# Kernel optimization log

Hardware: AMD Instinct MI355X
Metric: run time of the kernel (lower is better)

## Reference

```python
import jax, jax.numpy as jnp
import numpy as np
import math

B, NQ, HID = 1, 512, 4096
H, KVH, D = 32, 8, 128
NPRE, TOPK = 4096, 64
NREP = H // KVH


def _rope_tables(nq, d, base=10000.0):
    inv_freq = 1.0 / (base ** (np.arange(0, d, 2, dtype=np.float32) / d))
    freqs = np.outer(np.arange(nq, dtype=np.float32), inv_freq)  # [nq, d/2]
    emb = np.concatenate([freqs, freqs], axis=-1)                # [nq, d]
    return jnp.asarray(np.cos(emb))[None], jnp.asarray(np.sin(emb))[None]


def setup_inputs() -> dict:
    key = jax.random.key(0)
    ks = jax.random.split(key, 8)
    cos, sin = _rope_tables(NQ, D)
    wscale = 0.02
    return {
        "hidden_states": jax.random.normal(ks[0], (B, NQ, HID), jnp.float32),
        "cos": cos.astype(jnp.float32),
        "sin": sin.astype(jnp.float32),
        "prefix_key": jax.random.normal(ks[1], (B, KVH, NPRE, D), jnp.float32),
        "prefix_value": jax.random.normal(ks[2], (B, KVH, NPRE, D), jnp.float32),
        "Wq": jax.random.normal(ks[3], (HID, H * D), jnp.float32) * wscale,
        "Wk": jax.random.normal(ks[4], (HID, KVH * D), jnp.float32) * wscale,
        "Wv": jax.random.normal(ks[5], (HID, KVH * D), jnp.float32) * wscale,
        "Wo": jax.random.normal(ks[6], (H * D, HID), jnp.float32) * wscale,
    }


def _rotate_half(x):
    x1, x2 = jnp.split(x, 2, axis=-1)
    return jnp.concatenate([-x2, x1], axis=-1)


def _apply_rope(x, cos, sin):
    # x: [B, h, N, D]; cos/sin: [B, N, D] -> unsqueeze head dim (HF convention)
    c, s = cos[:, None], sin[:, None]
    return x * c + _rotate_half(x) * s


def _repeat_kv(x, n_rep):
    # [B, kvH, N, D] -> [B, kvH*n_rep, N, D] (repeat_interleave on head dim)
    b, kvh, n, d = x.shape
    return jnp.broadcast_to(x[:, :, None], (b, kvh, n_rep, n, d)).reshape(b, kvh * n_rep, n, d)


def reference(hidden_states, cos, sin, prefix_key, prefix_value, Wq, Wk, Wv, Wo):
    inv_sqrt_d = 1.0 / math.sqrt(D)

    q = (hidden_states @ Wq).reshape(B, NQ, H, D).transpose(0, 2, 1, 3)    # [B,H,Nq,D]
    k = (hidden_states @ Wk).reshape(B, NQ, KVH, D).transpose(0, 2, 1, 3)  # [B,kvH,Nq,D]
    v = (hidden_states @ Wv).reshape(B, NQ, KVH, D).transpose(0, 2, 1, 3)

    q = _apply_rope(q, cos, sin)
    k = _apply_rope(k, cos, sin)

    sk = _repeat_kv(k, NREP).reshape(B * H, NQ, D)            # suffix keys
    sv = _repeat_kv(v, NREP).reshape(B * H, NQ, D)            # suffix values
    pk = _repeat_kv(prefix_key, NREP).reshape(B * H, NPRE, D)  # FAISS DB keys (exact IP index)
    pv = _repeat_kv(prefix_value, NREP).reshape(B * H, NPRE, D)
    qf = q.reshape(B * H, NQ, D)

    # --- exact top-k inner-product search over prefix (== FAISS IndexFlatIP), scaled by 1/sqrt(D)
    prefix_scores = jnp.einsum('bnd,bmd->bnm', qf, pk) * inv_sqrt_d        # [BH,Nq,Npre]
    topk_values, topk_indices = jax.lax.top_k(prefix_scores, TOPK)         # [BH,Nq,k]

    topk_exp = jnp.exp(topk_values)
    topk_exp_sums = topk_exp.sum(axis=-1)                                  # [BH,Nq]

    # --- dense causal suffix attention (unnormalized, exp without max-shift, as in source)
    score_dense = jnp.einsum('bnd,bmd->bnm', qf, sk) * inv_sqrt_d          # [BH,Nq,Nq]
    causal = jnp.tril(jnp.ones((NQ, NQ), bool))
    score_dense = jnp.where(causal[None], score_dense, -jnp.inf)
    dense_exp = jnp.exp(score_dense)
    dense_exp_sums = dense_exp.sum(axis=-1)                                # [BH,Nq]

    denom = (topk_exp_sums + dense_exp_sums)[..., None]                    # shared softmax denom
    attn_topk = topk_exp / denom                                           # [BH,Nq,k]
    attn_dense = dense_exp / denom                                         # [BH,Nq,Nq]

    # --- sparse (COO) matmul with prefix values == gather + weighted sum
    bh_idx = jnp.arange(B * H)[:, None, None]
    gathered_pv = pv[bh_idx, topk_indices]                                 # [BH,Nq,k,D]
    xhat = jnp.einsum('bnk,bnkd->bnd', attn_topk, gathered_pv)
    xhat = xhat + attn_dense @ sv                                          # [BH,Nq,D]

    out = xhat.reshape(B, H, NQ, D).transpose(0, 2, 1, 3).reshape(B, NQ, H * D)
    return out @ Wo                                                        # [B,Nq,HID]
```

## Files before the change

### kernel.cpp

```cpp
#include <hip/hip_runtime.h>

#define DEV static __device__ __forceinline__

typedef _Float16 f16;
typedef __attribute__((ext_vector_type(8))) _Float16 f16x8;
typedef __attribute__((ext_vector_type(4))) _Float16 f16x4;
typedef __attribute__((ext_vector_type(4))) float    f32x4;

#define SCALE_QK 0.08838834764831845f

DEV float u2f(unsigned x){ union{unsigned u; float f;} c; c.u = x; return c.f; }

DEV void gload16(const f16* g, f16* l){
  __builtin_amdgcn_global_load_lds((const __attribute__((address_space(1))) void*)g,
                                   (__attribute__((address_space(3))) void*)l, 16, 0, 0);
}

template<int BM, int BN>
DEV void gemm_core3(const f16* At, int lda, const f16* Bt, int ldb, int K,
                    f32x4 (&acc)[BM/32][BN/32], f16* As, f16* Bs){
  constexpr int MR = BM / 32, NR = BN / 32;
  constexpr int ABUF = BM * 64, BBUF = BN * 64;
  static_assert(BM == 64 && BN == 64, "4 loads/wave/stage assumed");
  const int tid  = threadIdx.x;
  const int lane = tid & 63, w = tid >> 6;
  const int wr = w >> 1, wc = w & 1;
  const int lr = lane & 15, hi8 = (lane >> 4) * 8;
  const int srow = lane >> 3;
  const int sg   = (lane & 7) ^ srow;

  auto stage = [&](int buf, int k0){
#pragma unroll
    for (int i = 0; i < 2; ++i){
      const int ga = w + i * 4;
      gload16(At + (size_t)(ga * 8 + srow) * lda + k0 + sg * 8, As + buf * ABUF + ga * 512);
    }
#pragma unroll
    for (int i = 0; i < 2; ++i){
      const int gb = w + i * 4;
      gload16(Bt + (size_t)(gb * 8 + srow) * ldb + k0 + sg * 8, Bs + buf * BBUF + gb * 512);
    }
  };

  const int nt = K / 64;
  stage(0, 0);
  if (nt > 1) stage(1, 64);
  for (int t = 0; t < nt; ++t){
    if (t + 1 < nt) asm volatile("s_waitcnt vmcnt(4)" ::: "memory");
    else            asm volatile("s_waitcnt vmcnt(0)" ::: "memory");
    __builtin_amdgcn_sched_barrier(0);
    __builtin_amdgcn_s_barrier();
    __builtin_amdgcn_sched_barrier(0);
    const f16* Ab = As + (t % 3) * ABUF;
    const f16* Bb = Bs + (t % 3) * BBUF;
#pragma unroll
    for (int kk = 0; kk < 64; kk += 32){
      f16x8 a[MR], b[NR];
#pragma unroll
      for (int mi = 0; mi < MR; ++mi){
        const int row = wr * (BM / 2) + mi * 16 + lr;
        const int col = ((((kk + hi8) >> 3) ^ (row & 7)) << 3);
        a[mi] = *reinterpret_cast<const f16x8*>(&Ab[row * 64 + col]);
      }
#pragma unroll
      for (int ni = 0; ni < NR; ++ni){
        const int row = wc * (BN / 2) + ni * 16 + lr;
        const int col = ((((kk + hi8) >> 3) ^ (row & 7)) << 3);
        b[ni] = *reinterpret_cast<const f16x8*>(&Bb[row * 64 + col]);
      }
#pragma unroll
      for (int mi = 0; mi < MR; ++mi)
#pragma unroll
        for (int ni = 0; ni < NR; ++ni)
          acc[mi][ni] = __builtin_amdgcn_mfma_f32_16x16x32_f16(a[mi], b[ni], acc[mi][ni], 0, 0, 0);
    }
    if (t + 2 < nt) stage((t + 2) % 3, (t + 2) * 64);
  }
}

__global__ __launch_bounds__(256) void kcast(const float* __restrict__ in,
                                             f16* __restrict__ out, int n){
  int i = (blockIdx.x * 256 + threadIdx.x) * 4;
  if (i < n){
    f32x4 x = *reinterpret_cast<const f32x4*>(in + i);
    f16x4 y = { (f16)x[0], (f16)x[1], (f16)x[2], (f16)x[3] };
    *reinterpret_cast<f16x4*>(out + i) = y;
  }
}

__global__ __launch_bounds__(256) void ksplit(const float* __restrict__ in,
                                              f16* __restrict__ hi,
                                              f16* __restrict__ lo, int n4){
  int i = blockIdx.x * 256 + threadIdx.x;
  if (i < n4){
    f32x4 x = reinterpret_cast<const f32x4*>(in)[i];
    f16x4 h, l;
#pragma unroll
    for (int j = 0; j < 4; ++j){
      h[j] = (f16)x[j];
      l[j] = (f16)(x[j] - (float)h[j]);
    }
    reinterpret_cast<f16x4*>(hi)[i] = h;
    reinterpret_cast<f16x4*>(lo)[i] = l;
  }
}

__global__ __launch_bounds__(256) void ktransw(const float* __restrict__ in,
                                               f16* __restrict__ out, int R, int C){
  __shared__ float t[64][65];
  const int c0 = blockIdx.x * 64, r0 = blockIdx.y * 64;
  const int tx = threadIdx.x & 63, ty = threadIdx.x >> 6;
#pragma unroll
  for (int i = 0; i < 16; ++i)
    t[ty + i * 4][tx] = in[(size_t)(r0 + ty + i * 4) * C + c0 + tx];
  __syncthreads();
  const int rx = threadIdx.x & 15;
  const int cy = threadIdx.x >> 4;
#pragma unroll
  for (int i = 0; i < 4; ++i){
    const int cc = cy + i * 16;
    f16x4 v = { (f16)t[4 * rx + 0][cc], (f16)t[4 * rx + 1][cc],
                (f16)t[4 * rx + 2][cc], (f16)t[4 * rx + 3][cc] };
    *reinterpret_cast<f16x4*>(&out[(size_t)(c0 + cc) * R + r0 + rx * 4]) = v;
  }
}

__global__ __launch_bounds__(256) void ktrans3w(const float* __restrict__ Wq,
                                                const float* __restrict__ Wk,
                                                const float* __restrict__ Wv,
                                                f16* __restrict__ wqkvT){
  __shared__ float t[64][65];
  const int bx = blockIdx.x;
  const float* in; f16* out; int C, cx;
  if (bx < 64)      { in = Wq; out = wqkvT;                        C = 4096; cx = bx; }
  else if (bx < 80) { in = Wk; out = wqkvT + (size_t)4096 * 4096;  C = 1024; cx = bx - 64; }
  else              { in = Wv; out = wqkvT + (size_t)5120 * 4096;  C = 1024; cx = bx - 80; }
  const int c0 = cx * 64, r0 = blockIdx.y * 64;
  const int tx = threadIdx.x & 63, ty = threadIdx.x >> 6;
#pragma unroll
  for (int i = 0; i < 16; ++i)
    t[ty + i * 4][tx] = in[(size_t)(r0 + ty + i * 4) * C + c0 + tx];
  __syncthreads();
  const int rx = threadIdx.x & 15;
  const int cy = threadIdx.x >> 4;
#pragma unroll
  for (int i = 0; i < 4; ++i){
    const int cc = cy + i * 16;
    f16x4 v = { (f16)t[4 * rx + 0][cc], (f16)t[4 * rx + 1][cc],
                (f16)t[4 * rx + 2][cc], (f16)t[4 * rx + 3][cc] };
    *reinterpret_cast<f16x4*>(&out[(size_t)(c0 + cc) * 4096 + r0 + rx * 4]) = v;
  }
}

__global__ __launch_bounds__(256) void kgemm_qkv(const f16* __restrict__ A,
                                                 const f16* __restrict__ B,
                                                 float* __restrict__ qf,
                                                 float* __restrict__ kf,
                                                 f16* __restrict__ vbuf){
  __shared__ __align__(16) f16 As[3 * 64 * 64];
  __shared__ __align__(16) f16 Bs[3 * 64 * 64];
  const int orig = blockIdx.x + (blockIdx.y << 3);
  const int xcd = orig & 7, idx = orig >> 3;
  const int n_t = xcd * 12 + idx % 12;
  const int m_t = idx / 12;
  const int m0 = m_t * 64, n0 = n_t * 64;
  f32x4 acc[2][2];
#pragma unroll
  for (int i = 0; i < 2; ++i)
#pragma unroll
    for (int j = 0; j < 2; ++j){ f32x4 z = {0.f,0.f,0.f,0.f}; acc[i][j] = z; }
  gemm_core3<64,64>(A + (size_t)m0 * 4096, 4096, B + (size_t)n0 * 4096, 4096, 4096, acc, As, Bs);
  const int tid = threadIdx.x, lane = tid & 63, w = tid >> 6;
  const int wr = w >> 1, wc = w & 1, lr = lane & 15, hg = lane >> 4;
#pragma unroll
  for (int mi = 0; mi < 2; ++mi)
#pragma unroll
    for (int ni = 0; ni < 2; ++ni)
#pragma unroll
      for (int j = 0; j < 4; ++j){
        int rown = m0 + wr * 32 + mi * 16 + hg * 4 + j;
        int col  = n0 + wc * 32 + ni * 16 + lr;
        float vv = acc[mi][ni][j];
        if (col < 4096){
          int hh = col >> 7, dd = col & 127;
          qf[((size_t)hh * 512 + rown) * 128 + dd] = vv;
        } else if (col < 5120){
          int c2 = col - 4096; int hh = c2 >> 7, dd = c2 & 127;
          kf[((size_t)hh * 512 + rown) * 128 + dd] = vv;
        } else {
          int c2 = col - 5120; int hh = c2 >> 7, dd = c2 & 127;
          vbuf[((size_t)hh * 512 + rown) * 128 + dd] = (f16)vv;
        }
      }
}

__global__ __launch_bounds__(256) void krope_split(const float* __restrict__ qf,
                                                   const float* __restrict__ kf,
                                                   const float* __restrict__ cosb,
                                                   const float* __restrict__ sinb,
                                                   f16* __restrict__ qh, f16* __restrict__ ql,
                                                   f16* __restrict__ kh, f16* __restrict__ kl){
  int e = blockIdx.x * 256 + threadIdx.x;
  const int QP = 32 * 512 * 64;
  const float* src; f16 *oh, *ol; int e2;
  if (e < QP){ src = qf; oh = qh; ol = ql; e2 = e; }
  else       { src = kf; oh = kh; ol = kl; e2 = e - QP; }
  int rem = e2 & 32767, n = rem >> 6, d = rem & 63;
  size_t base = ((size_t)(e2 >> 15) * 512 + n) * 128;
  float x0 = src[base + d], x1 = src[base + d + 64];
  float c = cosb[n * 128 + d], s = sinb[n * 128 + d];
  float y0 = x0 * c - x1 * s;
  float y1 = x1 * c + x0 * s;
  f16 h0 = (f16)y0; oh[base + d]      = h0; ol[base + d]      = (f16)(y0 - (float)h0);
  f16 h1 = (f16)y1; oh[base + d + 64] = h1; ol[base + d + 64] = (f16)(y1 - (float)h1);
}

__global__ __launch_bounds__(256) void kgemm_score3(const f16* __restrict__ qh,
                                                    const f16* __restrict__ ql,
                                                    const f16* __restrict__ pkh,
                                                    const f16* __restrict__ pkl,
                                                    float* __restrict__ pscoreG,
                                                    int h0){
  __shared__ __align__(16) f16 Ah[128 * 64];
  __shared__ __align__(16) f16 Al[128 * 64];
  __shared__ __align__(16) f16 Bh[2 * 128 * 64];
  __shared__ __align__(16) f16 Bl[2 * 128 * 64];
  const int hl = blockIdx.z, h = h0 + hl, kvh = h >> 2;
  const int m0 = blockIdx.x * 128, n0 = blockIdx.y * 256;
  const f16* qhp = qh + ((size_t)h * 512 + m0) * 128;
  const f16* qlp = ql + ((size_t)h * 512 + m0) * 128;
  const f16* bhp = pkh + ((size_t)kvh * 4096 + n0) * 128;
  const f16* blp = pkl + ((size_t)kvh * 4096 + n0) * 128;
  f32x4 acc[2][4][4];
#pragma unroll
  for (int t = 0; t < 2; ++t)
#pragma unroll
    for (int i = 0; i < 4; ++i)
#pragma unroll
      for (int j = 0; j < 4; ++j){ f32x4 z = {0.f,0.f,0.f,0.f}; acc[t][i][j] = z; }

  const int tid  = threadIdx.x;
  const int lane = tid & 63, w = tid >> 6;
  const int wr = w >> 1, wc = w & 1;
  const int lr = lane & 15, hi8 = (lane >> 4) * 8;
  const int srow = lane >> 3;
  const int sg   = (lane & 7) ^ srow;

  for (int k0 = 0; k0 < 128; k0 += 64){
    __syncthreads();
#pragma unroll
    for (int i = 0; i < 4; ++i){
      const int q   = w * 4 + i;
      const int row = q * 8 + srow;
      const size_t go = (size_t)row * 128 + k0 + sg * 8;
      gload16(qhp + go, Ah + q * 512);
      gload16(qlp + go, Al + q * 512);
    }
    for (int i = w; i < 32; i += 4){
      const int row = i * 8 + srow;
      const size_t go = (size_t)row * 128 + k0 + sg * 8;
      gload16(bhp + go, Bh + i * 512);
      gload16(blp + go, Bl + i * 512);
    }
    __syncthreads();
#pragma unroll
    for (int kk = 0; kk < 64; kk += 32){
      f16x8 ah[4], al[4];
#pragma unroll
      for (int mi = 0; mi < 4; ++mi){
        const int row = wr * 64 + mi * 16 + lr;
        const int col = ((((kk + hi8) >> 3) ^ (row & 7)) << 3);
        ah[mi] = *reinterpret_cast<const f16x8*>(&Ah[row * 64 + col]);
        al[mi] = *reinterpret_cast<const f16x8*>(&Al[row * 64 + col]);
      }
#pragma unroll
      for (int t = 0; t < 2; ++t){
#pragma unroll
        for (int ni = 0; ni < 4; ++ni){
          const int rowb = t * 128 + wc * 64 + ni * 16 + lr;
          const int colb = ((((kk + hi8) >> 3) ^ (rowb & 7)) << 3);
          f16x8 bh = *reinterpret_cast<const f16x8*>(&Bh[rowb * 64 + colb]);
          f16x8 bl = *reinterpret_cast<const f16x8*>(&Bl[rowb * 64 + colb]);
#pragma unroll
          for (int mi = 0; mi < 4; ++mi){
            acc[t][mi][ni] = __builtin_amdgcn_mfma_f32_16x16x32_f16(ah[mi], bh, acc[t][mi][ni], 0, 0, 0);
            acc[t][mi][ni] = __builtin_amdgcn_mfma_f32_16x16x32_f16(ah[mi], bl, acc[t][mi][ni], 0, 0, 0);
            acc[t][mi][ni] = __builtin_amdgcn_mfma_f32_16x16x32_f16(al[mi], bh, acc[t][mi][ni], 0, 0, 0);
          }
        }
      }
    }
  }
  const int hg = lane >> 4;
#pragma unroll
  for (int t = 0; t < 2; ++t)
#pragma unroll
    for (int mi = 0; mi < 4; ++mi)
#pragma unroll
      for (int ni = 0; ni < 4; ++ni)
#pragma unroll
        for (int j = 0; j < 4; ++j){
          int rown = m0 + wr * 64 + mi * 16 + hg * 4 + j;
          int col  = n0 + t * 128 + wc * 64 + ni * 16 + lr;
          pscoreG[((size_t)hl * 512 + rown) * 4096 + col] = acc[t][mi][ni][j] * SCALE_QK;
        }
}

__global__ __launch_bounds__(256) void ktopk(const unsigned* __restrict__ pscoreG,
                                             const f16* __restrict__ pv16,
                                             float* __restrict__ xt,
                                             float* __restrict__ tsum,
                                             int h0){
  const int b = blockIdx.x;
  const int h = h0 + (b >> 9), kvh = h >> 2;
  const size_t hn = (size_t)h * 512 + (b & 511);
  __shared__ unsigned hist[256];
  __shared__ unsigned wtot[4];
  __shared__ unsigned wmax[4];
  __shared__ unsigned wtg[4], wte[4];
  __shared__ float    wred[4];
  __shared__ int   sidx[64];
  __shared__ float sw[64];
  __shared__ float red[256];
  __shared__ unsigned scal[2];
  const int tid = threadIdx.x, lane = tid & 63, wv = tid >> 6;
  const unsigned* rowp = pscoreG + ((size_t)b << 12) + tid * 16;
  unsigned key[16];
#pragma unroll
  for (int i = 0; i < 4; ++i)
    *reinterpret_cast<uint4*>(&key[i * 4]) = *reinterpret_cast<const uint4*>(&rowp[i * 4]);
#pragma unroll
  for (int k = 0; k < 16; ++k)
    key[k] = (key[k] & 0x80000000u) ? ~key[k] : (key[k] | 0x80000000u);

  unsigned pref, need;
  {
    unsigned mb = 0;
#pragma unroll
    for (int k = 0; k < 16; ++k) mb = max(mb, key[k] >> 24);
#pragma unroll
    for (int s2 = 32; s2 > 0; s2 >>= 1) mb = max(mb, (unsigned)__shfl_xor((int)mb, s2, 64));
    if (lane == 0) wmax[wv] = mb;
    __syncthreads();
    mb = max(max(wmax[0], wmax[1]), max(wmax[2], wmax[3]));
    __syncthreads();
    unsigned cum = 0, cur = mb;
    for (;;){
      unsigned cnt = 0, nxt = 0;
#pragma unroll
      for (int k = 0; k < 16; ++k){
        unsigned byte_ = key[k] >> 24;
        cnt += (byte_ == cur);
        if (byte_ < cur) nxt = max(nxt, byte_);
      }
#pragma unroll
      for (int s2 = 32; s2 > 0; s2 >>= 1){
        cnt += (unsigned)__shfl_xor((int)cnt, s2, 64);
        nxt  = max(nxt, (unsigned)__shfl_xor((int)nxt, s2, 64));
      }
      if (lane == 0){ wtot[wv] = cnt; wmax[wv] = nxt; }
      __syncthreads();
      unsigned tc = wtot[0] + wtot[1] + wtot[2] + wtot[3];
      unsigned tn = max(max(wmax[0], wmax[1]), max(wmax[2], wmax[3]));
      if (cum + tc >= 64u){ pref = cur; need = 64u - cum; break; }
      cum += tc; cur = tn;
      __syncthreads();
    }
    __syncthreads();
  }

#pragma unroll
  for (int lvl = 1; lvl < 3; ++lvl){
    const int sh = 24 - lvl * 8;
    hist[tid] = 0; __syncthreads();
#pragma unroll
    for (int k = 0; k < 16; ++k){
      if ((key[k] >> (sh + 8)) == pref) atomicAdd(&hist[(key[k] >> sh) & 255u], 1u);
    }
    __syncthreads();
    unsigned hval = hist[tid];
    unsigned sfx = hval;
#pragma unroll
    for (int s2 = 1; s2 < 64; s2 <<= 1){
      unsigned o = __shfl_down(sfx, s2, 64);
      if (lane + s2 < 64) sfx += o;
    }
    if (lane == 0) wtot[wv] = sfx;
    __syncthreads();
    unsigned add = 0;
#pragma unroll
    for (int w2 = 0; w2 < 4; ++w2) if (w2 > wv) add += wtot[w2];
    unsigned inc = sfx + add;
    unsigned abv = inc - hval;
    if (inc >= need && abv < need){ scal[0] = (unsigned)tid; scal[1] = need - abv; }
    __syncthreads();
    pref = (pref << 8) | scal[0];
    need = scal[1];
    __syncthreads();
  }
  const unsigned P = pref;

  int cgt = 0, ceq = 0;
#pragma unroll
  for (int k = 0; k < 16; ++k){
    unsigned t24 = key[k] >> 8;
    if (t24 > P) ++cgt; else if (t24 == P) ++ceq;
  }
  unsigned pg = (unsigned)cgt, pe = (unsigned)ceq;
#pragma unroll
  for (int s2 = 1; s2 < 64; s2 <<= 1){
    unsigned og_ = __shfl_up(pg, s2, 64);
    unsigned oe_ = __shfl_up(pe, s2, 64);
    if (lane >= s2){ pg += og_; pe += oe_; }
  }
  if (lane == 63){ wtg[wv] = pg; wte[wv] = pe; }
  __syncthreads();
  unsigned addg = 0, adde = 0, totg = 0;
#pragma unroll
  for (int w2 = 0; w2 < 4; ++w2){
    totg += wtg[w2];
    if (w2 < wv){ addg += wtg[w2]; adde += wte[w2]; }
  }
  const int totgt = (int)totg;
  const int slots = 64 - totgt;
  int og = (int)(pg + addg) - cgt;
  int oe = (int)(pe + adde) - ceq;
  float wsum = 0.f;
#pragma unroll
  for (int k = 0; k < 16; ++k){
    unsigned t24 = key[k] >> 8;
    unsigned orig = (key[k] & 0x80000000u) ? (key[k] & 0x7FFFFFFFu) : ~key[k];
    if (t24 > P){
      float e = __expf(u2f(orig));
      sidx[og] = tid * 16 + k; sw[og] = e; wsum += e; ++og;
    } else if (t24 == P){
      if (oe < slots){
        float e = __expf(u2f(orig));
        sidx[totgt + oe] = tid * 16 + k; sw[totgt + oe] = e; wsum += e;
      }
      ++oe;
    }
  }
#pragma unroll
  for (int s2 = 32; s2 > 0; s2 >>= 1) wsum += __shfl_xor(wsum, s2, 64);
  if (lane == 0) wred[wv] = wsum;
  __syncthreads();
  if (tid == 0) tsum[hn] = wred[0] + wred[1] + wred[2] + wred[3];

  const int d = tid & 127, half = tid >> 7;
  float acc = 0.f;
  const f16* pvb = pv16 + (size_t)kvh * 4096 * 128;
  for (int i = half * 32; i < half * 32 + 32; ++i)
    acc += sw[i] * (float)pvb[(size_t)sidx[i] * 128 + d];
  red[tid] = acc;
  __syncthreads();
  if (tid < 128) xt[hn * 128 + tid] = red[tid] + red[tid + 128];
}

__global__ __launch_bounds__(256) void kdense(const f16* __restrict__ qh,
                                              const f16* __restrict__ ql,
                                              const f16* __restrict__ kh,
                                              const f16* __restrict__ kl,
                                              const f16* __restrict__ v16,
                                              float* __restrict__ dsum,
                                              float* __restrict__ xd){
  const int ntile = blockIdx.x, h = blockIdx.y, kvh = h >> 2;
  const int n0 = ntile * 64;
  __shared__ __align__(16) f16 Ksh[64 * 136];
  __shared__ __align__(16) f16 Ksl[64 * 136];
  __shared__ __align__(16) f16 VT[128 * 72];
  __shared__ __align__(16) f16 Ps[64 * 72];
  const int tid = threadIdx.x, lane = tid & 63, w = tid >> 6;
  const int lr = lane & 15, hg = lane >> 4, hi8 = hg * 8;

  f16x8 aqh[4], aql[4];
  {
    const size_t qoff = ((size_t)h * 512 + n0 + w * 16 + lr) * 128;
#pragma unroll
    for (int c = 0; c < 4; ++c){
      aqh[c] = *reinterpret_cast<const f16x8*>(&qh[qoff + c * 32 + hi8]);
      aql[c] = *reinterpret_cast<const f16x8*>(&ql[qoff + c * 32 + hi8]);
    }
  }
  f32x4 o[8];
#pragma unroll
  for (int i = 0; i < 8; ++i){ f32x4 z = {0.f,0.f,0.f,0.f}; o[i] = z; }
  float dp[4] = {0.f, 0.f, 0.f, 0.f};

  for (int mt = 0; mt <= ntile; ++mt){
    const int m0 = mt * 64;
#pragma unroll
    for (int i = 0; i < 4; ++i){
      int vv = tid + i * 256; int row = vv >> 4, kc = (vv & 15) * 8;
      const size_t ko = ((size_t)kvh * 512 + m0 + row) * 128 + kc;
      *reinterpret_cast<f16x8*>(&Ksh[row * 136 + kc]) = *reinterpret_cast<const f16x8*>(&kh[ko]);
      *reinterpret_cast<f16x8*>(&Ksl[row * 136 + kc]) = *reinterpret_cast<const f16x8*>(&kl[ko]);
    }
#pragma unroll
    for (int i = 0; i < 8; ++i){
      int vv = tid + i * 256; int m = vv >> 5, d4 = (vv & 31) * 4;
      f16x4 x = *reinterpret_cast<const f16x4*>(&v16[((size_t)kvh * 512 + m0 + m) * 128 + d4]);
      VT[(d4 + 0) * 72 + m] = x[0];
      VT[(d4 + 1) * 72 + m] = x[1];
      VT[(d4 + 2) * 72 + m] = x[2];
      VT[(d4 + 3) * 72 + m] = x[3];
    }
    __syncthreads();
    f32x4 s[4];
#pragma unroll
    for (int j = 0; j < 4; ++j){ f32x4 z = {0.f,0.f,0.f,0.f}; s[j] = z; }
#pragma unroll
    for (int c = 0; c < 4; ++c){
#pragma unroll
      for (int j = 0; j < 4; ++j){
        f16x8 bkh = *reinterpret_cast<const f16x8*>(&Ksh[(j * 16 + lr) * 136 + c * 32 + hi8]);
        f16x8 bkl = *reinterpret_cast<const f16x8*>(&Ksl[(j * 16 + lr) * 136 + c * 32 + hi8]);
        s[j] = __builtin_amdgcn_mfma_f32_16x16x32_f16(aqh[c], bkh, s[j], 0, 0, 0);
        s[j] = __builtin_amdgcn_mfma_f32_16x16x32_f16(aqh[c], bkl, s[j], 0, 0, 0);
        s[j] = __builtin_amdgcn_mfma_f32_16x16x32_f16(aql[c], bkh, s[j], 0, 0, 0);
      }
    }
#pragma unroll
    for (int j = 0; j < 4; ++j)
#pragma unroll
      for (int r = 0; r < 4; ++r){
        int ng = n0 + w * 16 + hg * 4 + r;
        int mg = m0 + j * 16 + lr;
        float p = (mg <= ng) ? __expf(s[j][r] * SCALE_QK) : 0.f;
        dp[r] += p;
        Ps[(w * 16 + hg * 4 + r) * 72 + j * 16 + lr] = (f16)p;
      }
    __syncthreads();
#pragma unroll
    for (int kk = 0; kk < 64; kk += 32){
      f16x8 pa = *reinterpret_cast<const f16x8*>(&Ps[(w * 16 + lr) * 72 + kk + hi8]);
#pragma unroll
      for (int dt = 0; dt < 8; ++dt){
        f16x8 bv = *reinterpret_cast<const f16x8*>(&VT[(dt * 16 + lr) * 72 + kk + hi8]);
        o[dt] = __builtin_amdgcn_mfma_f32_16x16x32_f16(pa, bv, o[dt], 0, 0, 0);
      }
    }
    __syncthreads();
  }
#pragma unroll
  for (int r = 0; r < 4; ++r){
    float vs = dp[r];
#pragma unroll
    for (int off2 = 1; off2 < 16; off2 <<= 1) vs += __shfl_xor(vs, off2, 64);
    if (lr == 0) dsum[h * 512 + n0 + w * 16 + hg * 4 + r] = vs;
  }
#pragma unroll
  for (int dt = 0; dt < 8; ++dt)
#pragma unroll
    for (int r = 0; r < 4; ++r){
      int ng = n0 + w * 16 + hg * 4 + r;
      xd[((size_t)h * 512 + ng) * 128 + dt * 16 + lr] = o[dt][r];
    }
}

__global__ __launch_bounds__(256) void kcombine(const float* __restrict__ xt,
                                                const float* __restrict__ xd,
                                                const float* __restrict__ tsum,
                                                const float* __restrict__ dsum,
                                                f16* __restrict__ xh16){
  int e = blockIdx.x * 256 + threadIdx.x;
  int hn = e >> 7, d = e & 127;
  int h = hn >> 9, n = hn & 511;
  float denom = tsum[hn] + dsum[hn];
  float v = (xt[e] + xd[e]) / denom;
  xh16[(size_t)n * 4096 + h * 128 + d] = (f16)v;
}

__global__ __launch_bounds__(256) void kgemm_out(const f16* __restrict__ A,
                                                 const f16* __restrict__ B,
                                                 float* __restrict__ out){
  __shared__ __align__(16) f16 As[3 * 64 * 64];
  __shared__ __align__(16) f16 Bs[3 * 64 * 64];
  const int orig = blockIdx.x + (blockIdx.y << 3);
  const int xcd = orig & 7, idx = orig >> 3;
  const int n_t = xcd * 8 + idx % 8;
  const int m_t = idx / 8;
  const int m0 = m_t * 64, n0 = n_t * 64;
  f32x4 acc[2][2];
#pragma unroll
  for (int i = 0; i < 2; ++i)
#pragma unroll
    for (int j = 0; j < 2; ++j){ f32x4 z = {0.f,0.f,0.f,0.f}; acc[i][j] = z; }
  gemm_core3<64,64>(A + (size_t)m0 * 4096, 4096, B + (size_t)n0 * 4096, 4096, 4096, acc, As, Bs);
  const int tid = threadIdx.x, lane = tid & 63, w = tid >> 6;
  const int wr = w >> 1, wc = w & 1, lr = lane & 15, hg = lane >> 4;
#pragma unroll
  for (int mi = 0; mi < 2; ++mi)
#pragma unroll
    for (int ni = 0; ni < 2; ++ni)
#pragma unroll
      for (int j = 0; j < 4; ++j){
        int rown = m0 + wr * 32 + mi * 16 + hg * 4 + j;
        int col  = n0 + wc * 32 + ni * 16 + lr;
        out[(size_t)rown * 4096 + col] = acc[mi][ni][j];
      }
}

extern "C" void kernel_launch(void* const* d_in, const int* in_sizes, int n_in,
                              void* d_out, int out_size, void* d_ws, size_t ws_size,
                              hipStream_t stream){
  (void)in_sizes; (void)n_in; (void)out_size;
  const float* hs   = (const float*)d_in[0];
  const float* cosb = (const float*)d_in[1];
  const float* sinb = (const float*)d_in[2];
  const float* pk   = (const float*)d_in[3];
  const float* pv   = (const float*)d_in[4];
  const float* Wq   = (const float*)d_in[5];
  const float* Wk   = (const float*)d_in[6];
  const float* Wv   = (const float*)d_in[7];
  const float* Wo   = (const float*)d_in[8];
  float* out = (float*)d_out;

  char* ws = (char*)d_ws;
  size_t off = 0;
  auto alloc = [&](size_t bytes) -> void* {
    void* p = ws + off; off += (bytes + 255) & ~(size_t)255; return p;
  };
  f16*  h16    = (f16*)alloc((size_t)512 * 4096 * 2);
  f16*  wqkvT  = (f16*)alloc((size_t)6144 * 4096 * 2);
  f16*  pkh    = (f16*)alloc((size_t)8 * 4096 * 128 * 2);
  f16*  pkl    = (f16*)alloc((size_t)8 * 4096 * 128 * 2);
  f16*  pv16   = (f16*)alloc((size_t)8 * 4096 * 128 * 2);
  f16*  v16    = (f16*)alloc((size_t)8 * 512 * 128 * 2);
  f16*  qhh    = (f16*)alloc((size_t)32 * 512 * 128 * 2);
  f16*  qll    = (f16*)alloc((size_t)32 * 512 * 128 * 2);
  f16*  khh    = (f16*)alloc((size_t)8 * 512 * 128 * 2);
  f16*  kll    = (f16*)alloc((size_t)8 * 512 * 128 * 2);
  float* xd    = (float*)alloc((size_t)32 * 512 * 128 * 4);
  float* qf32  = (float*)alloc((size_t)32 * 512 * 128 * 4);
  float* kf32  = (float*)alloc((size_t)8 * 512 * 128 * 4);

  f16*   woT     = wqkvT;
  float* xt      = qf32;
  float* tsum    = kf32;
  float* dsum    = kf32 + 32 * 512;
  f16*   xh16    = h16;

  const size_t bigBytes = (size_t)8 * 512 * 4096 * 4;
  const bool   big      = (ws_size >= off + bigBytes + 256);
  float* pscoreUse = big ? (float*)(ws + off) : (float*)wqkvT;
  const int hN = big ? 8 : 4;

  kcast<<<2048, 256, 0, stream>>>(hs, h16, 512 * 4096);
  ksplit<<<4096, 256, 0, stream>>>(pk, pkh, pkl, 8 * 4096 * 128 / 4);
  kcast<<<4096, 256, 0, stream>>>(pv, pv16, 8 * 4096 * 128);
  ktrans3w<<<dim3(96, 64), 256, 0, stream>>>(Wq, Wk, Wv, wqkvT);

  kgemm_qkv<<<dim3(8, 96), 256, 0, stream>>>(h16, wqkvT, qf32, kf32, v16);
  krope_split<<<5120, 256, 0, stream>>>(qf32, kf32, cosb, sinb, qhh, qll, khh, kll);

  for (int h0 = 0; h0 < 32; h0 += hN){
    kgemm_score3<<<dim3(4, 16, hN), 256, 0, stream>>>(qhh, qll, pkh, pkl, pscoreUse, h0);
    ktopk<<<hN * 512, 256, 0, stream>>>((const unsigned*)pscoreUse, pv16, xt, tsum, h0);
  }

  ktransw<<<dim3(64, 64), 256, 0, stream>>>(Wo, woT, 4096, 4096);

  kdense<<<dim3(8, 32), 256, 0, stream>>>(qhh, qll, khh, kll, v16, dsum, xd);
  kcombine<<<8192, 256, 0, stream>>>(xt, xd, tsum, dsum, xh16);
  kgemm_out<<<dim3(8, 64), 256, 0, stream>>>(xh16, woT, out);
}
```

Before: 381.1 us.

## Use 512-thread score GEMM blocks and gather fp32 prefix values directly

```diff
diff --git a/kernel.cpp b/kernel.cpp
--- a/kernel.cpp
+++ b/kernel.cpp
@@ -215,7 +215,7 @@
   f16 h1 = (f16)y1; oh[base + d + 64] = h1; ol[base + d + 64] = (f16)(y1 - (float)h1);
 }
 
-__global__ __launch_bounds__(256) void kgemm_score3(const f16* __restrict__ qh,
+__global__ __launch_bounds__(512) void kgemm_score3(const f16* __restrict__ qh,
                                                     const f16* __restrict__ ql,
                                                     const f16* __restrict__ pkh,
                                                     const f16* __restrict__ pkl,
@@ -231,32 +231,28 @@
   const f16* qlp = ql + ((size_t)h * 512 + m0) * 128;
   const f16* bhp = pkh + ((size_t)kvh * 4096 + n0) * 128;
   const f16* blp = pkl + ((size_t)kvh * 4096 + n0) * 128;
-  f32x4 acc[2][4][4];
-#pragma unroll
-  for (int t = 0; t < 2; ++t)
-#pragma unroll
-    for (int i = 0; i < 4; ++i)
-#pragma unroll
-      for (int j = 0; j < 4; ++j){ f32x4 z = {0.f,0.f,0.f,0.f}; acc[t][i][j] = z; }
+  f32x4 acc[4][4];
+#pragma unroll
+  for (int i = 0; i < 4; ++i)
+#pragma unroll
+    for (int j = 0; j < 4; ++j){ f32x4 z = {0.f,0.f,0.f,0.f}; acc[i][j] = z; }
 
   const int tid  = threadIdx.x;
   const int lane = tid & 63, w = tid >> 6;
-  const int wr = w >> 1, wc = w & 1;
+  const int wr = w >> 2, wc = w & 3;
   const int lr = lane & 15, hi8 = (lane >> 4) * 8;
   const int srow = lane >> 3;
   const int sg   = (lane & 7) ^ srow;
 
   for (int k0 = 0; k0 < 128; k0 += 64){
     __syncthreads();
-#pragma unroll
-    for (int i = 0; i < 4; ++i){
-      const int q   = w * 4 + i;
-      const int row = q * 8 + srow;
+    for (int i = w; i < 16; i += 8){
+      const int row = i * 8 + srow;
       const size_t go = (size_t)row * 128 + k0 + sg * 8;
-      gload16(qhp + go, Ah + q * 512);
-      gload16(qlp + go, Al + q * 512);
-    }
-    for (int i = w; i < 32; i += 4){
+      gload16(qhp + go, Ah + i * 512);
+      gload16(qlp + go, Al + i * 512);
+    }
+    for (int i = w; i < 32; i += 8){
       const int row = i * 8 + srow;
       const size_t go = (size_t)row * 128 + k0 + sg * 8;
       gload16(bhp + go, Bh + i * 512);
@@ -274,40 +270,35 @@
         al[mi] = *reinterpret_cast<const f16x8*>(&Al[row * 64 + col]);
       }
 #pragma unroll
-      for (int t = 0; t < 2; ++t){
-#pragma unroll
-        for (int ni = 0; ni < 4; ++ni){
-          const int rowb = t * 128 + wc * 64 + ni * 16 + lr;
-          const int colb = ((((kk + hi8) >> 3) ^ (rowb & 7)) << 3);
-          f16x8 bh = *reinterpret_cast<const f16x8*>(&Bh[rowb * 64 + colb]);
-          f16x8 bl = *reinterpret_cast<const f16x8*>(&Bl[rowb * 64 + colb]);
-#pragma unroll
-          for (int mi = 0; mi < 4; ++mi){
-            acc[t][mi][ni] = __builtin_amdgcn_mfma_f32_16x16x32_f16(ah[mi], bh, acc[t][mi][ni], 0, 0, 0);
-            acc[t][mi][ni] = __builtin_amdgcn_mfma_f32_16x16x32_f16(ah[mi], bl, acc[t][mi][ni], 0, 0, 0);
-            acc[t][mi][ni] = __builtin_amdgcn_mfma_f32_16x16x32_f16(al[mi], bh, acc[t][mi][ni], 0, 0, 0);
-          }
+      for (int ni = 0; ni < 4; ++ni){
+        const int rowb = wc * 64 + ni * 16 + lr;
+        const int colb = ((((kk + hi8) >> 3) ^ (rowb & 7)) << 3);
+        f16x8 bh = *reinterpret_cast<const f16x8*>(&Bh[rowb * 64 + colb]);
+        f16x8 bl = *reinterpret_cast<const f16x8*>(&Bl[rowb * 64 + colb]);
+#pragma unroll
+        for (int mi = 0; mi < 4; ++mi){
+          acc[mi][ni] = __builtin_amdgcn_mfma_f32_16x16x32_f16(ah[mi], bh, acc[mi][ni], 0, 0, 0);
+          acc[mi][ni] = __builtin_amdgcn_mfma_f32_16x16x32_f16(ah[mi], bl, acc[mi][ni], 0, 0, 0);
+          acc[mi][ni] = __builtin_amdgcn_mfma_f32_16x16x32_f16(al[mi], bh, acc[mi][ni], 0, 0, 0);
         }
       }
     }
   }
   const int hg = lane >> 4;
 #pragma unroll
-  for (int t = 0; t < 2; ++t)
-#pragma unroll
-    for (int mi = 0; mi < 4; ++mi)
-#pragma unroll
-      for (int ni = 0; ni < 4; ++ni)
-#pragma unroll
-        for (int j = 0; j < 4; ++j){
-          int rown = m0 + wr * 64 + mi * 16 + hg * 4 + j;
-          int col  = n0 + t * 128 + wc * 64 + ni * 16 + lr;
-          pscoreG[((size_t)hl * 512 + rown) * 4096 + col] = acc[t][mi][ni][j] * SCALE_QK;
-        }
+  for (int mi = 0; mi < 4; ++mi)
+#pragma unroll
+    for (int ni = 0; ni < 4; ++ni)
+#pragma unroll
+      for (int j = 0; j < 4; ++j){
+        int rown = m0 + wr * 64 + mi * 16 + hg * 4 + j;
+        int col  = n0 + wc * 64 + ni * 16 + lr;
+        pscoreG[((size_t)hl * 512 + rown) * 4096 + col] = acc[mi][ni][j] * SCALE_QK;
+      }
 }
 
 __global__ __launch_bounds__(256) void ktopk(const unsigned* __restrict__ pscoreG,
-                                             const f16* __restrict__ pv16,
+                                             const float* __restrict__ pvf,
                                              float* __restrict__ xt,
                                              float* __restrict__ tsum,
                                              int h0){
@@ -449,9 +440,9 @@
 
   const int d = tid & 127, half = tid >> 7;
   float acc = 0.f;
-  const f16* pvb = pv16 + (size_t)kvh * 4096 * 128;
+  const float* pvb = pvf + (size_t)kvh * 4096 * 128;
   for (int i = half * 32; i < half * 32 + 32; ++i)
-    acc += sw[i] * (float)pvb[(size_t)sidx[i] * 128 + d];
+    acc += sw[i] * pvb[(size_t)sidx[i] * 128 + d];
   red[tid] = acc;
   __syncthreads();
   if (tid < 128) xt[hn * 128 + tid] = red[tid] + red[tid + 128];
@@ -625,7 +616,6 @@
   f16*  wqkvT  = (f16*)alloc((size_t)6144 * 4096 * 2);
   f16*  pkh    = (f16*)alloc((size_t)8 * 4096 * 128 * 2);
   f16*  pkl    = (f16*)alloc((size_t)8 * 4096 * 128 * 2);
-  f16*  pv16   = (f16*)alloc((size_t)8 * 4096 * 128 * 2);
   f16*  v16    = (f16*)alloc((size_t)8 * 512 * 128 * 2);
   f16*  qhh    = (f16*)alloc((size_t)32 * 512 * 128 * 2);
   f16*  qll    = (f16*)alloc((size_t)32 * 512 * 128 * 2);
@@ -648,15 +638,14 @@
 
   kcast<<<2048, 256, 0, stream>>>(hs, h16, 512 * 4096);
   ksplit<<<4096, 256, 0, stream>>>(pk, pkh, pkl, 8 * 4096 * 128 / 4);
-  kcast<<<4096, 256, 0, stream>>>(pv, pv16, 8 * 4096 * 128);
   ktrans3w<<<dim3(96, 64), 256, 0, stream>>>(Wq, Wk, Wv, wqkvT);
 
   kgemm_qkv<<<dim3(8, 96), 256, 0, stream>>>(h16, wqkvT, qf32, kf32, v16);
   krope_split<<<5120, 256, 0, stream>>>(qf32, kf32, cosb, sinb, qhh, qll, khh, kll);
 
   for (int h0 = 0; h0 < 32; h0 += hN){
-    kgemm_score3<<<dim3(4, 16, hN), 256, 0, stream>>>(qhh, qll, pkh, pkl, pscoreUse, h0);
-    ktopk<<<hN * 512, 256, 0, stream>>>((const unsigned*)pscoreUse, pv16, xt, tsum, h0);
+    kgemm_score3<<<dim3(4, 16, hN), 512, 0, stream>>>(qhh, qll, pkh, pkl, pscoreUse, h0);
+    ktopk<<<hN * 512, 256, 0, stream>>>((const unsigned*)pscoreUse, pv, xt, tsum, h0);
   }
 
   ktransw<<<dim3(64, 64), 256, 0, stream>>>(Wo, woT, 4096, 4096);
```

Result: no change. 375.4 us (-1.5%).
